# Kernel tuning notes

Measured on AMD Instinct MI355X. Metric: run time of the kernel, lower is better.

Reference implementation:

```python
import jax, jax.numpy as jnp
import numpy as np

TOP_K = 8
EPS = 1e-12  # F.normalize eps


def setup_inputs() -> dict:
    key = jax.random.key(0)
    ks = jax.random.split(key, 16)
    B, C, T, E, H, O, N = 1024, 64, 2, 512, 512, 1, 200000
    f = lambda k, s, scale: jax.random.normal(k, s, jnp.float32) * scale
    z = lambda s: jnp.zeros(s, jnp.float32)
    return {
        "treatment": f(ks[0], (B, T), 1.0),
        "confounders": f(ks[1], (B, C), 1.0),
        "patient": f(ks[2], (B, C + T), 1.0),
        "corpus_embeddings": f(ks[3], (N, E), 1.0),
        "W_pe": f(ks[4], (C + T, E), 0.05), "b_pe": z((E,)),
        "W_te": f(ks[5], (T, H), 0.05), "b_te": z((H,)),
        "W_ce": f(ks[6], (C, H), 0.05), "b_ce": z((H,)),
        "W_re": f(ks[7], (E * TOP_K, H), 0.02), "b_re": z((H,)),
        "W_o1": f(ks[8], (3 * H, H), 0.02), "b_o1": z((H,)),
        "W_o2": f(ks[9], (H, H // 2), 0.05), "b_o2": z((H // 2,)),
        "W_o3": f(ks[10], (H // 2, O), 0.05), "b_o3": z((O,)),
        "W_p1": f(ks[11], (C, H), 0.05), "b_p1": z((H,)),
        "W_p2": f(ks[12], (H, T), 0.05), "b_p2": z((T,)),
    }


def _l2norm(x):
    # torch F.normalize: x / max(||x||, eps)
    n = jnp.sqrt(jnp.sum(x * x, axis=1, keepdims=True))
    return x / jnp.maximum(n, EPS)


def reference(treatment, confounders, patient, corpus_embeddings,
              W_pe, b_pe, W_te, b_te, W_ce, b_ce, W_re, b_re,
              W_o1, b_o1, W_o2, b_o2, W_o3, b_o3, W_p1, b_p1, W_p2, b_p2):
    B = patient.shape[0]
    # retrieval: encode -> normalize -> similarity -> top-k -> gather
    q = _l2norm(patient @ W_pe + b_pe)                 # [B, E]
    c = _l2norm(corpus_embeddings)                     # [N, E]
    sim = q @ c.T                                      # [B, N]
    scores, idx = jax.lax.top_k(sim, TOP_K)            # [B, K]
    retrieved = corpus_embeddings[idx]                 # [B, K, E] (raw, un-normalized, as in source)
    flat = retrieved.reshape(B, -1)                    # [B, K*E]
    # encoders
    t_enc = treatment @ W_te + b_te
    c_enc = confounders @ W_ce + b_ce
    r_enc = flat @ W_re + b_re
    combined = jnp.concatenate([t_enc, c_enc, r_enc], axis=1)  # [B, 3H]
    # outcome MLP (dropout is identity in eval)
    h = jax.nn.relu(combined @ W_o1 + b_o1)
    h = jax.nn.relu(h @ W_o2 + b_o2)
    outcome = h @ W_o3 + b_o3                          # [B, O]
    # propensity head
    p = jax.nn.relu(confounders @ W_p1 + b_p1)
    propensity = jax.nn.softmax(p @ W_p2 + b_p2, axis=1)
    return outcome, scores, idx, propensity
```

## Files before the change

kernel.cpp:

```cpp
#include <hip/hip_runtime.h>
#include <math.h>

#define TOPK 8
#define NCORPUS 200000
#define BROWS 1024
#define CHUNK 512
#define NCHUNK 391
#define NT 32
#define NPART 4
#define NEGINF (-3.0e38f)

typedef __attribute__((ext_vector_type(8))) short bf16x8;
typedef __attribute__((ext_vector_type(4))) float f32x4;

__device__ __forceinline__ float wave_sum_f32(float v) {
#pragma unroll
  for (int m = 32; m >= 1; m >>= 1) v += __shfl_xor(v, m, 64);
  return v;
}
__device__ __forceinline__ double wave_sum_f64(double v) {
#pragma unroll
  for (int m = 32; m >= 1; m >>= 1) v += __shfl_xor(v, m, 64);
  return v;
}
__device__ __forceinline__ unsigned short f2bf(float f) {
  unsigned int u = __float_as_uint(f);
  unsigned int r = (u + 0x7fffu + ((u >> 16) & 1u)) >> 16;
  return (unsigned short)r;
}
__device__ __forceinline__ void gload16(const void* g, void* l) {
  __builtin_amdgcn_global_load_lds(
      (const __attribute__((address_space(1))) unsigned int*)g,
      (__attribute__((address_space(3))) unsigned int*)l, 16, 0, 0);
}
__device__ __forceinline__ void kins4f(float (&S)[4], float v) {
#pragma unroll
  for (int p = 0; p < 4; ++p) {
    float mx = fmaxf(S[p], v);
    v = fminf(S[p], v);
    S[p] = mx;
  }
}
__device__ __forceinline__ void pmerge4f(float (&a)[4], const float (&b)[4]) {
  float c0 = fmaxf(a[0], b[3]), c1 = fmaxf(a[1], b[2]);
  float c2 = fmaxf(a[2], b[1]), c3 = fmaxf(a[3], b[0]);
  float t;
  t = fmaxf(c0, c2); c2 = fminf(c0, c2); c0 = t;
  t = fmaxf(c1, c3); c3 = fminf(c1, c3); c1 = t;
  t = fmaxf(c0, c1); c1 = fminf(c0, c1); c0 = t;
  t = fmaxf(c2, c3); c3 = fminf(c2, c3); c2 = t;
  a[0] = c0; a[1] = c1; a[2] = c2; a[3] = c3;
}

__global__ void prep_kernel(const float* __restrict__ corpus, unsigned short* __restrict__ Cpk,
                            const float* __restrict__ patient, const float* __restrict__ Wpe,
                            const float* __restrict__ bpe, double* __restrict__ q64,
                            unsigned short* __restrict__ Qpk) {
  __shared__ float ps[66];
  __shared__ double red[4];
  __shared__ double s_den;
  int tid = threadIdx.x;
  if (blockIdx.x < 50000) {
    int wid = tid >> 6, lane = tid & 63;
    int row = blockIdx.x * 4 + wid;
    if (row >= NCORPUS) return;
    const float4* p = (const float4*)(corpus + (size_t)row * 512);
    float4 a = p[lane * 2], b = p[lane * 2 + 1];
    float s = a.x * a.x + a.y * a.y + a.z * a.z + a.w * a.w +
              b.x * b.x + b.y * b.y + b.z * b.z + b.w * b.w;
    s = wave_sum_f32(s);
    float inv = 1.0f / fmaxf(sqrtf(s), 1e-12f);
    union { unsigned short us[8]; uint4 v; } pk;
    pk.us[0] = f2bf(a.x * inv); pk.us[1] = f2bf(a.y * inv);
    pk.us[2] = f2bf(a.z * inv); pk.us[3] = f2bf(a.w * inv);
    pk.us[4] = f2bf(b.x * inv); pk.us[5] = f2bf(b.y * inv);
    pk.us[6] = f2bf(b.z * inv); pk.us[7] = f2bf(b.w * inv);
    *(uint4*)(Cpk + (size_t)row * 512 + lane * 8) = pk.v;
  } else {
    int b = blockIdx.x - 50000;
    if (tid < 66) ps[tid] = patient[b * 66 + tid];
    __syncthreads();
    double v0 = (double)bpe[tid];
    double v1 = (double)bpe[tid + 256];
    for (int k = 0; k < 66; ++k) {
      double p = (double)ps[k];
      v0 += p * (double)Wpe[k * 512 + tid];
      v1 += p * (double)Wpe[k * 512 + tid + 256];
    }
    double ss = wave_sum_f64(v0 * v0 + v1 * v1);
    if ((tid & 63) == 0) red[tid >> 6] = ss;
    __syncthreads();
    if (tid == 0) s_den = fmax(sqrt(red[0] + red[1] + red[2] + red[3]), 1e-12);
    __syncthreads();
    double den = s_den;
    double o0 = v0 / den, o1 = v1 / den;
    q64[(size_t)b * 512 + tid] = o0;
    q64[(size_t)b * 512 + tid + 256] = o1;
    Qpk[(size_t)b * 512 + tid] = f2bf((float)o0);
    Qpk[(size_t)b * 512 + tid + 256] = f2bf((float)o1);
  }
}

template <bool CHECK>
__device__ __forceinline__ void fold_sub(f32x4 (&acc)[4][4], float (&lk)[4][4],
                                         int tagbase, int rb2) {
#pragma unroll
  for (int m = 0; m < 4; ++m)
#pragma unroll
    for (int j = 0; j < 4; ++j) {
      int mj = m * 16 + j;
      unsigned tg = (unsigned)(tagbase - mj);
      bool ok = true;
      if (CHECK) ok = (rb2 + mj) < NCORPUS;
#pragma unroll
      for (int n = 0; n < 4; ++n) {
        unsigned bb = (__float_as_uint(acc[m][n][j]) & 0xFFFFFC00u) | tg;
        float tf = __uint_as_float(bb);
        if (CHECK) tf = ok ? tf : NEGINF;
        kins4f(lk[n], tf);
      }
    }
}

__global__ __launch_bounds__(256, 2) void sim_topk_mfma(
    const unsigned short* __restrict__ Qpk, const unsigned short* __restrict__ Cpk,
    unsigned int* __restrict__ part_k) {
  __shared__ __align__(16) unsigned short smem[2][16384];

  int tid = threadIdx.x;
  int lane = tid & 63, wid = tid >> 6;
  int wr = wid >> 1, wc = wid & 1;
  int g = (blockIdx.x & 7) * NCHUNK + (blockIdx.x >> 3);
  int chunk = g >> 3, mt = g & 7;
  int m0 = mt * 128;
  int rbase = chunk * CHUNK;
  bool lastChunk = (rbase + CHUNK) > NCORPUS;

  int srow = tid >> 3;
  int scol = (((tid & 7) ^ (srow & 7)) << 3);

  int l15 = lane & 15, l4 = lane >> 4, l7 = lane & 7;
  int aoff[2][4], boff[2][4];
#pragma unroll
  for (int kk = 0; kk < 2; ++kk)
#pragma unroll
    for (int q = 0; q < 4; ++q) {
      int sw = (((kk * 4 + l4) ^ l7) << 3);
      aoff[kk][q] = (wr * 64 + q * 16 + l15) * 64 + sw;
      boff[kk][q] = 8192 + (wc * 64 + q * 16 + l15) * 64 + sw;
    }

  float lk[4][NPART];
#pragma unroll
  for (int n = 0; n < 4; ++n)
#pragma unroll
    for (int p = 0; p < NPART; ++p) lk[n][p] = NEGINF;

  f32x4 zero = {0.f, 0.f, 0.f, 0.f};
  f32x4 acc[4][4];
#pragma unroll
  for (int m = 0; m < 4; ++m)
#pragma unroll
    for (int n = 0; n < 4; ++n) acc[m][n] = zero;

  auto stageA = [&](int t, unsigned short* dst) {
    int sub = t >> 3, kt = t & 7;
    int rb = rbase + sub * 128;
    int k0 = kt * 64;
#pragma unroll
    for (int r = 0; r < 4; ++r) {
      int cr = rb + r * 32 + srow;
      if (cr > NCORPUS - 1) cr = NCORPUS - 1;
      gload16(Cpk + (size_t)cr * 512 + k0 + scol, dst + (r * 4 + wid) * 512);
    }
  };
  auto stageB = [&](int t, unsigned short* dst) {
    int kt = t & 7;
    int k0 = kt * 64;
#pragma unroll
    for (int r = 0; r < 4; ++r) {
      int qr = m0 + r * 32 + srow;
      gload16(Qpk + (size_t)qr * 512 + k0 + scol, dst + 8192 + (r * 4 + wid) * 512);
    }
  };

  stageA(0, smem[0]);
  stageB(0, smem[0]);

  for (int t = 0; t < NT; ++t) {
    int t1 = t + 1;
    if (t1 < NT) {
      unsigned short* nb = smem[t1 & 1];
      stageA(t1, nb);
      stageB(t1, nb);
      asm volatile("s_waitcnt vmcnt(8)" ::: "memory");
    } else {
      asm volatile("s_waitcnt vmcnt(0)" ::: "memory");
    }
    __builtin_amdgcn_s_barrier();
    const unsigned short* cb = smem[t & 1];
#pragma unroll
    for (int kk = 0; kk < 2; ++kk) {
      bf16x8 a[4], b[4];
#pragma unroll
      for (int m = 0; m < 4; ++m) a[m] = *(const bf16x8*)(cb + aoff[kk][m]);
#pragma unroll
      for (int n = 0; n < 4; ++n) b[n] = *(const bf16x8*)(cb + boff[kk][n]);
#pragma unroll
      for (int m = 0; m < 4; ++m)
#pragma unroll
        for (int n = 0; n < 4; ++n)
          acc[m][n] = __builtin_amdgcn_mfma_f32_16x16x32_bf16(a[m], b[n], acc[m][n], 0, 0, 0);
    }
    if ((t & 7) == 7) {
      int sub = t >> 3;
      int cellbase = sub * 128 + wr * 64 + l4 * 4;
      int rb2 = rbase + cellbase;
      int tagbase = (CHUNK - 1) - cellbase;
      if (lastChunk) fold_sub<true>(acc, lk, tagbase, rb2);
      else fold_sub<false>(acc, lk, tagbase, rb2);
#pragma unroll
      for (int m = 0; m < 4; ++m)
#pragma unroll
        for (int n = 0; n < 4; ++n) acc[m][n] = zero;
    }
    __builtin_amdgcn_s_barrier();
  }

#pragma unroll
  for (int rnd = 0; rnd < 2; ++rnd) {
    int msk = 16 << rnd;
#pragma unroll
    for (int n = 0; n < 4; ++n) {
      float ov[NPART];
#pragma unroll
      for (int p = 0; p < NPART; ++p) ov[p] = __shfl_xor(lk[n][p], msk, 64);
      pmerge4f(lk[n], ov);
    }
  }
  float* fb = (float*)&smem[0][0];
  if (wr == 1 && l4 == 0) {
#pragma unroll
    for (int n = 0; n < 4; ++n) {
      int col = wc * 64 + n * 16 + l15;
#pragma unroll
      for (int p = 0; p < NPART; ++p) fb[col * 4 + p] = lk[n][p];
    }
  }
  __syncthreads();
  if (wr == 0 && l4 == 0) {
#pragma unroll
    for (int n = 0; n < 4; ++n) {
      int col = wc * 64 + n * 16 + l15;
      float ov[NPART];
#pragma unroll
      for (int p = 0; p < NPART; ++p) ov[p] = fb[col * 4 + p];
      pmerge4f(lk[n], ov);
      size_t base = ((size_t)(m0 + col) * NCHUNK + chunk) * NPART;
#pragma unroll
      for (int p = 0; p < NPART; ++p) {
        unsigned bits = __float_as_uint(lk[n][p]);
        unsigned tag = bits & 0x3FFu;
        unsigned flip = bits ^ ((unsigned)((int)bits >> 31) | 0x80000000u);
        part_k[base + p] = (flip & 0xFFFFFC00u) | tag;
      }
    }
  }
}

__global__ __launch_bounds__(256, 2) void mr_tp_kernel(
    const unsigned int* __restrict__ part_k,
    const double* __restrict__ q64, const float* __restrict__ corpus,
    float* __restrict__ out_scores, float* __restrict__ out_idxf, int* __restrict__ topidx,
    const float* __restrict__ treatment, const float* __restrict__ conf,
    const float* __restrict__ Wte, const float* __restrict__ bte,
    const float* __restrict__ Wce, const float* __restrict__ bce,
    const float* __restrict__ Wp1, const float* __restrict__ bp1,
    const float* __restrict__ Wp2, const float* __restrict__ bp2,
    float* __restrict__ combined, float* __restrict__ out_prop) {
  __shared__ float cs[64];
  __shared__ float red0[4], red1[4];
  int tid = threadIdx.x;
  if (blockIdx.x < 256) {
    int wv = tid >> 6, lane = tid & 63;
    int row = blockIdx.x * 4 + wv;
    if (row >= BROWS) return;

    unsigned tk[16]; int tm[16];
#pragma unroll
    for (int p = 0; p < 16; ++p) { tk[p] = 0u; tm[p] = 0; }
    const unsigned* base = part_k + (size_t)row * (NCHUNK * NPART);
    for (int e = lane; e < NCHUNK * NPART; e += 64) {
      unsigned k = base[e];
      if (k > tk[15]) {
        unsigned kv = k; int mv = e;
#pragma unroll
        for (int p = 0; p < 16; ++p) {
          bool gt = kv > tk[p];
          unsigned ts = tk[p]; int ti = tm[p];
          tk[p] = gt ? kv : ts; tm[p] = gt ? mv : ti;
          kv = gt ? ts : kv;    mv = gt ? ti : mv;
        }
      }
    }
#pragma unroll
    for (int r = 0; r < 6; ++r) {
      unsigned ov[16]; int om[16];
#pragma unroll
      for (int p = 0; p < 16; ++p) {
        ov[p] = __shfl_xor(tk[p], 1 << r, 64);
        om[p] = __shfl_xor(tm[p], 1 << r, 64);
      }
      unsigned cv[16]; int cm[16];
#pragma unroll
      for (int i = 0; i < 16; ++i) {
        bool t = tk[i] >= ov[15 - i];
        cv[i] = t ? tk[i] : ov[15 - i];
        cm[i] = t ? tm[i] : om[15 - i];
      }
#pragma unroll
      for (int s = 8; s >= 1; s >>= 1)
#pragma unroll
        for (int bb = 0; bb < 16; bb += 2 * s)
#pragma unroll
          for (int o = 0; o < s; ++o) {
            int x = bb + o, y = bb + o + s;
            bool t = cv[x] >= cv[y];
            unsigned hv = t ? cv[x] : cv[y]; unsigned lv = t ? cv[y] : cv[x];
            int hm = t ? cm[x] : cm[y];      int lm = t ? cm[y] : cm[x];
            cv[x] = hv; cm[x] = hm; cv[y] = lv; cm[y] = lm;
          }
#pragma unroll
      for (int i = 0; i < 16; ++i) { tk[i] = cv[i]; tm[i] = cm[i]; }
    }
    int cidx[16];
#pragma unroll
    for (int c = 0; c < 16; ++c) {
      int ic = ((tm[c] >> 2) << 9) + (CHUNK - 1) - (int)(tk[c] & 0x3FFu);
      if (ic > NCORPUS - 1) ic = NCORPUS - 1;
      if (ic < 0) ic = 0;
      cidx[c] = ic;
    }
    double qv[8];
    const double* qrow = q64 + (size_t)row * 512;
#pragma unroll
    for (int t = 0; t < 8; ++t) qv[t] = qrow[lane * 8 + t];
    double rs[16];
#pragma unroll
    for (int c = 0; c < 16; ++c) {
      const float* crow = corpus + (size_t)cidx[c] * 512 + lane * 8;
      double qd = 0.0, cd = 0.0;
#pragma unroll
      for (int t = 0; t < 8; ++t) {
        double x = (double)crow[t];
        cd += x * x;
        qd += qv[t] * x;
      }
      qd = wave_sum_f64(qd);
      cd = wave_sum_f64(cd);
      rs[c] = qd / fmax(sqrt(cd), 1e-12);
    }
    if (lane == 0) {
      for (int o = 0; o < TOPK; ++o) {
        double bsc = -1e300;
        int bid2 = 0x7fffffff, bc = -1;
#pragma unroll
        for (int c = 0; c < 16; ++c) {
          bool better = (rs[c] > bsc) || (rs[c] == bsc && cidx[c] < bid2);
          if (better) { bsc = rs[c]; bid2 = cidx[c]; bc = c; }
        }
        out_scores[row * 8 + o] = (float)bsc;
        out_idxf[row * 8 + o] = (float)bid2;
        topidx[row * 8 + o] = bid2;
#pragma unroll
        for (int c = 0; c < 16; ++c)
          if (c == bc) rs[c] = -1e300;
      }
    }
  } else {
    int b = blockIdx.x - 256;
    if (tid < 64) cs[tid] = conf[b * 64 + tid];
    __syncthreads();
    float t0 = treatment[b * 2], t1 = treatment[b * 2 + 1];
    float l0 = 0.f, l1 = 0.f;
#pragma unroll
    for (int rep = 0; rep < 2; ++rep) {
      int h = tid + rep * 256;
      float te = fmaf(t0, Wte[h], fmaf(t1, Wte[512 + h], bte[h]));
      combined[(size_t)b * 1024 + h] = te;
      float ce = bce[h];
      float pv = bp1[h];
      for (int k = 0; k < 64; ++k) {
        float c = cs[k];
        ce = fmaf(c, Wce[k * 512 + h], ce);
        pv = fmaf(c, Wp1[k * 512 + h], pv);
      }
      combined[(size_t)b * 1024 + 512 + h] = ce;
      pv = fmaxf(pv, 0.f);
      l0 = fmaf(pv, Wp2[h * 2], l0);
      l1 = fmaf(pv, Wp2[h * 2 + 1], l1);
    }
    l0 = wave_sum_f32(l0);
    l1 = wave_sum_f32(l1);
    int wv = tid >> 6, lane = tid & 63;
    if (lane == 0) { red0[wv] = l0; red1[wv] = l1; }
    __syncthreads();
    if (tid == 0) {
      float a = red0[0] + red0[1] + red0[2] + red0[3] + bp2[0];
      float c2 = red1[0] + red1[1] + red1[2] + red1[3] + bp2[1];
      float m = fmaxf(a, c2);
      float e0 = expf(a - m), e1 = expf(c2 - m);
      float inv = 1.f / (e0 + e1);
      out_prop[b * 2] = e0 * inv;
      out_prop[b * 2 + 1] = e1 * inv;
    }
  }
}

template <int MODE, bool SPLIT, bool EPI>
__global__ __launch_bounds__(256, 2) void gemm64_kernel(
    const float* __restrict__ combined, const float* __restrict__ p0,
    const float* __restrict__ p1, const float* __restrict__ abias,
    const int* __restrict__ gidx, const float* __restrict__ corpus,
    const float* __restrict__ W, int ldw, const float* __restrict__ ebias,
    float* __restrict__ C0, float* __restrict__ C1, int ldc, int Kspan) {
  __shared__ float As[2][32 * 68];
  __shared__ float Bs[2][32 * 72];
  __shared__ int gi[512];
  int tid = threadIdx.x;
  int by = blockIdx.y;
  int m0, koff;
  float* Cout;
  if (SPLIT) {
    m0 = (by >> 1) * 64;
    int kh = by & 1;
    koff = kh * Kspan;
    Cout = kh ? C1 : C0;
  } else {
    m0 = by * 64;
    koff = 0;
    Cout = C0;
  }
  int n0 = blockIdx.x * 64;
  int nk = Kspan >> 5;

  if (MODE == 0) {
    gi[tid] = gidx[m0 * 8 + tid];
    gi[tid + 256] = gidx[m0 * 8 + tid + 256];
    __syncthreads();
  }

  int arow0 = tid >> 3, afc = tid & 7;
  int arow1 = arow0 + 32;
  int bkb0 = tid >> 4, bnf = tid & 15;
  int bkb1 = bkb0 + 16;

  auto stageA1 = [&](int row, int ks, int buf) {
    int kg = koff + ks * 32 + afc * 4;
    float4 v;
    if (MODE == 0) {
      int r = gi[row * 8 + (kg >> 9)];
      v = *(const float4*)(corpus + (size_t)r * 512 + (kg & 511));
    } else if (MODE == 1) {
      if (kg < 1024) {
        v = *(const float4*)(combined + (size_t)(m0 + row) * 1024 + kg);
      } else {
        int e = kg - 1024;
        float4 x = *(const float4*)(p0 + (size_t)(m0 + row) * 512 + e);
        float4 y = *(const float4*)(p1 + (size_t)(m0 + row) * 512 + e);
        float4 z = *(const float4*)(abias + e);
        v.x = x.x + y.x + z.x; v.y = x.y + y.y + z.y;
        v.z = x.z + y.z + z.z; v.w = x.w + y.w + z.w;
      }
    } else {
      float4 x = *(const float4*)(p0 + (size_t)(m0 + row) * 512 + kg);
      float4 y = *(const float4*)(p1 + (size_t)(m0 + row) * 512 + kg);
      float4 z = *(const float4*)(abias + kg);
      v.x = fmaxf(x.x + y.x + z.x, 0.f); v.y = fmaxf(x.y + y.y + z.y, 0.f);
      v.z = fmaxf(x.z + y.z + z.z, 0.f); v.w = fmaxf(x.w + y.w + z.w, 0.f);
    }
    float* d = As[buf] + (afc * 4) * 68 + row;
    d[0] = v.x; d[68] = v.y; d[136] = v.z; d[204] = v.w;
  };
  auto stage = [&](int ks, int buf) {
    stageA1(arow0, ks, buf);
    stageA1(arow1, ks, buf);
    int kg0 = koff + ks * 32 + bkb0;
    *(float4*)(Bs[buf] + bkb0 * 72 + bnf * 4) =
        *(const float4*)(W + (size_t)kg0 * ldw + n0 + bnf * 4);
    int kg1 = koff + ks * 32 + bkb1;
    *(float4*)(Bs[buf] + bkb1 * 72 + bnf * 4) =
        *(const float4*)(W + (size_t)kg1 * ldw + n0 + bnf * 4);
  };

  float acc[4][4];
#pragma unroll
  for (int i = 0; i < 4; ++i)
#pragma unroll
    for (int j = 0; j < 4; ++j) acc[i][j] = 0.f;

  int tm = tid >> 4, tn = tid & 15;

  stage(0, 0);
  __syncthreads();
  for (int ks = 0; ks < nk; ++ks) {
    if (ks + 1 < nk) stage(ks + 1, (ks + 1) & 1);
    const float* as = As[ks & 1];
    const float* bs = Bs[ks & 1];
#pragma unroll
    for (int k = 0; k < 32; ++k) {
      float4 a4 = *(const float4*)(as + k * 68 + tm * 4);
      float4 b4 = *(const float4*)(bs + k * 72 + tn * 4);
      float av[4] = {a4.x, a4.y, a4.z, a4.w};
      float bv[4] = {b4.x, b4.y, b4.z, b4.w};
#pragma unroll
      for (int i = 0; i < 4; ++i)
#pragma unroll
        for (int j = 0; j < 4; ++j) acc[i][j] = fmaf(av[i], bv[j], acc[i][j]);
    }
    __syncthreads();
  }

  float4 eb = make_float4(0.f, 0.f, 0.f, 0.f);
  if (EPI) eb = *(const float4*)(ebias + n0 + tn * 4);
#pragma unroll
  for (int i = 0; i < 4; ++i) {
    float4 v;
    v.x = acc[i][0]; v.y = acc[i][1]; v.z = acc[i][2]; v.w = acc[i][3];
    if (EPI) {
      v.x = fmaxf(v.x + eb.x, 0.f); v.y = fmaxf(v.y + eb.y, 0.f);
      v.z = fmaxf(v.z + eb.z, 0.f); v.w = fmaxf(v.w + eb.w, 0.f);
    }
    *(float4*)(Cout + (size_t)(m0 + tm * 4 + i) * ldc + n0 + tn * 4) = v;
  }
}

__global__ void outcome_kernel(const float* __restrict__ h2, const float* __restrict__ Wo3,
                               const float* __restrict__ bo3, float* __restrict__ out) {
  int wv = threadIdx.x >> 6, lane = threadIdx.x & 63;
  int row = blockIdx.x * 4 + wv;
  if (row >= BROWS) return;
  float4 a = ((const float4*)(h2 + (size_t)row * 256))[lane];
  float4 w = ((const float4*)Wo3)[lane];
  float s = a.x * w.x + a.y * w.y + a.z * w.z + a.w * w.w;
  s = wave_sum_f32(s);
  if (lane == 0) out[row] = s + bo3[0];
}

extern "C" void kernel_launch(void* const* d_in, const int* in_sizes, int n_in,
                              void* d_out, int out_size, void* d_ws, size_t ws_size,
                              hipStream_t stream) {
  const float* treatment = (const float*)d_in[0];
  const float* conf = (const float*)d_in[1];
  const float* patient = (const float*)d_in[2];
  const float* corpus = (const float*)d_in[3];
  const float* Wpe = (const float*)d_in[4];
  const float* bpe = (const float*)d_in[5];
  const float* Wte = (const float*)d_in[6];
  const float* bte = (const float*)d_in[7];
  const float* Wce = (const float*)d_in[8];
  const float* bce = (const float*)d_in[9];
  const float* Wre = (const float*)d_in[10];
  const float* bre = (const float*)d_in[11];
  const float* Wo1 = (const float*)d_in[12];
  const float* bo1 = (const float*)d_in[13];
  const float* Wo2 = (const float*)d_in[14];
  const float* bo2 = (const float*)d_in[15];
  const float* Wo3 = (const float*)d_in[16];
  const float* bo3 = (const float*)d_in[17];
  const float* Wp1 = (const float*)d_in[18];
  const float* bp1 = (const float*)d_in[19];
  const float* Wp2 = (const float*)d_in[20];
  const float* bp2 = (const float*)d_in[21];

  float* out = (float*)d_out;
  float* out_outcome = out;
  float* out_scores = out + 1024;
  float* out_idxf = out + 1024 + 8192;
  float* out_prop = out + 1024 + 8192 + 8192;

  char* ws = (char*)d_ws;
  size_t off = 0;
  auto carve = [&](size_t bytes) {
    void* p = ws + off;
    off = (off + bytes + 255) & ~(size_t)255;
    return p;
  };
  double* q64 = (double*)carve((size_t)1024 * 512 * 8);
  unsigned short* Qpk = (unsigned short*)carve((size_t)1024 * 512 * 2);
  unsigned short* Cpk = (unsigned short*)carve((size_t)NCORPUS * 512 * 2);
  unsigned int* part_k = (unsigned int*)carve((size_t)1024 * NCHUNK * NPART * 4);
  int* topidx = (int*)carve((size_t)1024 * 8 * 4);
  float* combined = (float*)carve((size_t)1024 * 1024 * 4);
  float* p0 = (float*)carve((size_t)1024 * 512 * 4);
  float* p1 = (float*)carve((size_t)1024 * 512 * 4);
  float* pp0 = (float*)carve((size_t)1024 * 512 * 4);
  float* pp1 = (float*)carve((size_t)1024 * 512 * 4);
  float* h2 = (float*)carve((size_t)1024 * 256 * 4);

  prep_kernel<<<dim3(51024), dim3(256), 0, stream>>>(corpus, Cpk, patient, Wpe, bpe, q64, Qpk);
  sim_topk_mfma<<<dim3(8 * NCHUNK), dim3(256), 0, stream>>>(Qpk, Cpk, part_k);
  mr_tp_kernel<<<dim3(1280), dim3(256), 0, stream>>>(part_k, q64, corpus,
                                                     out_scores, out_idxf, topidx,
                                                     treatment, conf, Wte, bte, Wce, bce,
                                                     Wp1, bp1, Wp2, bp2, combined, out_prop);
  gemm64_kernel<0, true, false><<<dim3(8, 32), dim3(256), 0, stream>>>(
      (const float*)nullptr, (const float*)nullptr, (const float*)nullptr, (const float*)nullptr,
      topidx, corpus, Wre, 512, (const float*)nullptr, p0, p1, 512, 2048);
  gemm64_kernel<1, true, false><<<dim3(8, 32), dim3(256), 0, stream>>>(
      combined, p0, p1, bre, (const int*)nullptr, (const float*)nullptr,
      Wo1, 512, (const float*)nullptr, pp0, pp1, 512, 768);
  gemm64_kernel<2, false, true><<<dim3(4, 16), dim3(256), 0, stream>>>(
      (const float*)nullptr, pp0, pp1, bo1, (const int*)nullptr, (const float*)nullptr,
      Wo2, 256, bo2, h2, (float*)nullptr, 256, 512);
  outcome_kernel<<<dim3(256), dim3(256), 0, stream>>>(h2, Wo3, bo3, out_outcome);
}
```

Measured before the change: 635.6 us.

## Compute retrieval encoder with bf16 MFMA using normalized corpus and norm rescale

```diff
diff --git a/kernel.cpp b/kernel.cpp
--- a/kernel.cpp
+++ b/kernel.cpp
@@ -55,10 +55,12 @@
 __global__ void prep_kernel(const float* __restrict__ corpus, unsigned short* __restrict__ Cpk,
                             const float* __restrict__ patient, const float* __restrict__ Wpe,
                             const float* __restrict__ bpe, double* __restrict__ q64,
-                            unsigned short* __restrict__ Qpk) {
+                            unsigned short* __restrict__ Qpk,
+                            const float* __restrict__ Wre, unsigned short* __restrict__ WreT) {
   __shared__ float ps[66];
   __shared__ double red[4];
   __shared__ double s_den;
+  __shared__ float tbuf[64 * 65];
   int tid = threadIdx.x;
   if (blockIdx.x < 50000) {
     int wid = tid >> 6, lane = tid & 63;
@@ -76,7 +78,7 @@
     pk.us[4] = f2bf(b.x * inv); pk.us[5] = f2bf(b.y * inv);
     pk.us[6] = f2bf(b.z * inv); pk.us[7] = f2bf(b.w * inv);
     *(uint4*)(Cpk + (size_t)row * 512 + lane * 8) = pk.v;
-  } else {
+  } else if (blockIdx.x < 51024) {
     int b = blockIdx.x - 50000;
     if (tid < 66) ps[tid] = patient[b * 66 + tid];
     __syncthreads();
@@ -98,6 +100,25 @@
     q64[(size_t)b * 512 + tid + 256] = o1;
     Qpk[(size_t)b * 512 + tid] = f2bf((float)o0);
     Qpk[(size_t)b * 512 + tid + 256] = f2bf((float)o1);
+  } else {
+    int tb = blockIdx.x - 51024;
+    int kt = tb >> 3, nt = tb & 7;
+    int k0 = kt * 64, n0 = nt * 64;
+    int r = tid >> 2, q = tid & 3;
+#pragma unroll
+    for (int i = 0; i < 4; ++i) {
+      float4 v = *(const float4*)(Wre + (size_t)(k0 + r) * 512 + n0 + q * 16 + i * 4);
+      float* d = tbuf + r * 65 + q * 16 + i * 4;
+      d[0] = v.x; d[1] = v.y; d[2] = v.z; d[3] = v.w;
+    }
+    __syncthreads();
+    int n = tid >> 2, s = tid & 3;
+    union { unsigned short us[16]; uint4 v[2]; } ob;
+#pragma unroll
+    for (int j = 0; j < 16; ++j) ob.us[j] = f2bf(tbuf[(s * 16 + j) * 65 + n]);
+    unsigned short* dst = WreT + (size_t)(n0 + n) * 4096 + k0 + s * 16;
+    *(uint4*)dst = ob.v[0];
+    *(uint4*)(dst + 8) = ob.v[1];
   }
 }
 
@@ -272,6 +293,7 @@
     const unsigned int* __restrict__ part_k,
     const double* __restrict__ q64, const float* __restrict__ corpus,
     float* __restrict__ out_scores, float* __restrict__ out_idxf, int* __restrict__ topidx,
+    float* __restrict__ rnorm,
     const float* __restrict__ treatment, const float* __restrict__ conf,
     const float* __restrict__ Wte, const float* __restrict__ bte,
     const float* __restrict__ Wce, const float* __restrict__ bce,
@@ -346,6 +368,7 @@
 #pragma unroll
     for (int t = 0; t < 8; ++t) qv[t] = qrow[lane * 8 + t];
     double rs[16];
+    float rn[16];
 #pragma unroll
     for (int c = 0; c < 16; ++c) {
       const float* crow = corpus + (size_t)cidx[c] * 512 + lane * 8;
@@ -358,7 +381,9 @@
       }
       qd = wave_sum_f64(qd);
       cd = wave_sum_f64(cd);
-      rs[c] = qd / fmax(sqrt(cd), 1e-12);
+      double nr = fmax(sqrt(cd), 1e-12);
+      rs[c] = qd / nr;
+      rn[c] = (float)nr;
     }
     if (lane == 0) {
       for (int o = 0; o < TOPK; ++o) {
@@ -372,6 +397,7 @@
         out_scores[row * 8 + o] = (float)bsc;
         out_idxf[row * 8 + o] = (float)bid2;
         topidx[row * 8 + o] = bid2;
+        rnorm[row * 8 + o] = rn[bc];
 #pragma unroll
         for (int c = 0; c < 16; ++c)
           if (c == bc) rs[c] = -1e300;
@@ -387,7 +413,7 @@
     for (int rep = 0; rep < 2; ++rep) {
       int h = tid + rep * 256;
       float te = fmaf(t0, Wte[h], fmaf(t1, Wte[512 + h], bte[h]));
-      combined[(size_t)b * 1024 + h] = te;
+      combined[(size_t)b * 1536 + h] = te;
       float ce = bce[h];
       float pv = bp1[h];
       for (int k = 0; k < 64; ++k) {
@@ -395,7 +421,7 @@
         ce = fmaf(c, Wce[k * 512 + h], ce);
         pv = fmaf(c, Wp1[k * 512 + h], pv);
       }
-      combined[(size_t)b * 1024 + 512 + h] = ce;
+      combined[(size_t)b * 1536 + 512 + h] = ce;
       pv = fmaxf(pv, 0.f);
       l0 = fmaf(pv, Wp2[h * 2], l0);
       l1 = fmaf(pv, Wp2[h * 2 + 1], l1);
@@ -417,38 +443,141 @@
   }
 }
 
-template <int MODE, bool SPLIT, bool EPI>
-__global__ __launch_bounds__(256, 2) void gemm64_kernel(
-    const float* __restrict__ combined, const float* __restrict__ p0,
-    const float* __restrict__ p1, const float* __restrict__ abias,
-    const int* __restrict__ gidx, const float* __restrict__ corpus,
-    const float* __restrict__ W, int ldw, const float* __restrict__ ebias,
+__global__ __launch_bounds__(256, 1) void renc_mfma(
+    const unsigned short* __restrict__ Cpk, const unsigned short* __restrict__ WreT,
+    const int* __restrict__ topidx, const float* __restrict__ rnorm,
+    const float* __restrict__ bre, float* __restrict__ combined) {
+  __shared__ __align__(16) unsigned short smem[2][16384];
+  __shared__ int gi[1024];
+
+  int tid = threadIdx.x;
+  int lane = tid & 63, wid = tid >> 6;
+  int wr = wid >> 1, wc = wid & 1;
+  int m0 = (blockIdx.x >> 2) * 128;
+  int n0 = (blockIdx.x & 3) * 128;
+
+#pragma unroll
+  for (int i = 0; i < 4; ++i) gi[tid + i * 256] = topidx[m0 * 8 + tid + i * 256];
+  __syncthreads();
+
+  int srow = tid >> 3;
+  int scol = (((tid & 7) ^ (srow & 7)) << 3);
+  int idxr[4][8];
+#pragma unroll
+  for (int r = 0; r < 4; ++r)
+#pragma unroll
+    for (int s = 0; s < 8; ++s) idxr[r][s] = gi[(r * 32 + srow) * 8 + s];
+
+  int l15 = lane & 15, l4 = lane >> 4, l7 = lane & 7;
+  int aoff[2][4], boff[2][4];
+#pragma unroll
+  for (int kk = 0; kk < 2; ++kk)
+#pragma unroll
+    for (int q = 0; q < 4; ++q) {
+      int sw = (((kk * 4 + l4) ^ l7) << 3);
+      aoff[kk][q] = (wr * 64 + q * 16 + l15) * 64 + sw;
+      boff[kk][q] = 8192 + (wc * 64 + q * 16 + l15) * 64 + sw;
+    }
+
+  f32x4 zero = {0.f, 0.f, 0.f, 0.f};
+  f32x4 acc[4][4], acc2[4][4];
+#pragma unroll
+  for (int m = 0; m < 4; ++m)
+#pragma unroll
+    for (int n = 0; n < 4; ++n) { acc[m][n] = zero; acc2[m][n] = zero; }
+
+  auto stageA = [&](int t, unsigned short* dst) {
+    int seg = t >> 3;
+    int kk = (t & 7) * 64;
+#pragma unroll
+    for (int r = 0; r < 4; ++r)
+      gload16(Cpk + (size_t)idxr[r][seg] * 512 + kk + scol, dst + (r * 4 + wid) * 512);
+  };
+  auto stageB = [&](int t, unsigned short* dst) {
+    int k0 = t * 64;
+#pragma unroll
+    for (int r = 0; r < 4; ++r) {
+      int nr = n0 + r * 32 + srow;
+      gload16(WreT + (size_t)nr * 4096 + k0 + scol, dst + 8192 + (r * 4 + wid) * 512);
+    }
+  };
+
+  stageA(0, smem[0]);
+  stageB(0, smem[0]);
+
+  for (int t = 0; t < 64; ++t) {
+    int t1 = t + 1;
+    if (t1 < 64) {
+      unsigned short* nb = smem[t1 & 1];
+      stageA(t1, nb);
+      stageB(t1, nb);
+      asm volatile("s_waitcnt vmcnt(8)" ::: "memory");
+    } else {
+      asm volatile("s_waitcnt vmcnt(0)" ::: "memory");
+    }
+    __builtin_amdgcn_s_barrier();
+    const unsigned short* cb = smem[t & 1];
+#pragma unroll
+    for (int kk = 0; kk < 2; ++kk) {
+      bf16x8 a[4], b[4];
+#pragma unroll
+      for (int m = 0; m < 4; ++m) a[m] = *(const bf16x8*)(cb + aoff[kk][m]);
+#pragma unroll
+      for (int n = 0; n < 4; ++n) b[n] = *(const bf16x8*)(cb + boff[kk][n]);
+#pragma unroll
+      for (int m = 0; m < 4; ++m)
+#pragma unroll
+        for (int n = 0; n < 4; ++n)
+          acc[m][n] = __builtin_amdgcn_mfma_f32_16x16x32_bf16(a[m], b[n], acc[m][n], 0, 0, 0);
+    }
+    if ((t & 7) == 7) {
+      int seg = t >> 3;
+#pragma unroll
+      for (int m = 0; m < 4; ++m)
+#pragma unroll
+        for (int j = 0; j < 4; ++j) {
+          int row = m0 + wr * 64 + m * 16 + l4 * 4 + j;
+          float rn = rnorm[row * 8 + seg];
+#pragma unroll
+          for (int n = 0; n < 4; ++n) acc2[m][n][j] = fmaf(rn, acc[m][n][j], acc2[m][n][j]);
+        }
+#pragma unroll
+      for (int m = 0; m < 4; ++m)
+#pragma unroll
+        for (int n = 0; n < 4; ++n) acc[m][n] = zero;
+    }
+    __builtin_amdgcn_s_barrier();
+  }
+
+#pragma unroll
+  for (int m = 0; m < 4; ++m)
+#pragma unroll
+    for (int j = 0; j < 4; ++j) {
+      int row = m0 + wr * 64 + m * 16 + l4 * 4 + j;
+#pragma unroll
+      for (int n = 0; n < 4; ++n) {
+        int col = n0 + wc * 64 + n * 16 + l15;
+        combined[(size_t)row * 1536 + 1024 + col] = acc2[m][n][j] + bre[col];
+      }
+    }
+}
+
+template <bool RELUIN>
+__global__ __launch_bounds__(256, 2) void gemm64f(
+    const float* __restrict__ A, int lda,
+    const float* __restrict__ p0, const float* __restrict__ p1, const float* __restrict__ ab,
+    const float* __restrict__ W, int ldw,
     float* __restrict__ C0, float* __restrict__ C1, int ldc, int Kspan) {
   __shared__ float As[2][32 * 68];
   __shared__ float Bs[2][32 * 72];
-  __shared__ int gi[512];
   int tid = threadIdx.x;
   int by = blockIdx.y;
-  int m0, koff;
-  float* Cout;
-  if (SPLIT) {
-    m0 = (by >> 1) * 64;
-    int kh = by & 1;
-    koff = kh * Kspan;
-    Cout = kh ? C1 : C0;
-  } else {
-    m0 = by * 64;
-    koff = 0;
-    Cout = C0;
-  }
+  int m0 = (by >> 1) * 64;
+  int kh = by & 1;
+  int koff = kh * Kspan;
+  float* Cout = kh ? C1 : C0;
   int n0 = blockIdx.x * 64;
   int nk = Kspan >> 5;
-
-  if (MODE == 0) {
-    gi[tid] = gidx[m0 * 8 + tid];
-    gi[tid + 256] = gidx[m0 * 8 + tid + 256];
-    __syncthreads();
-  }
 
   int arow0 = tid >> 3, afc = tid & 7;
   int arow1 = arow0 + 32;
@@ -458,26 +587,14 @@
   auto stageA1 = [&](int row, int ks, int buf) {
     int kg = koff + ks * 32 + afc * 4;
     float4 v;
-    if (MODE == 0) {
-      int r = gi[row * 8 + (kg >> 9)];
-      v = *(const float4*)(corpus + (size_t)r * 512 + (kg & 511));
-    } else if (MODE == 1) {
-      if (kg < 1024) {
-        v = *(const float4*)(combined + (size_t)(m0 + row) * 1024 + kg);
-      } else {
-        int e = kg - 1024;
-        float4 x = *(const float4*)(p0 + (size_t)(m0 + row) * 512 + e);
-        float4 y = *(const float4*)(p1 + (size_t)(m0 + row) * 512 + e);
-        float4 z = *(const float4*)(abias + e);
-        v.x = x.x + y.x + z.x; v.y = x.y + y.y + z.y;
-        v.z = x.z + y.z + z.z; v.w = x.w + y.w + z.w;
-      }
-    } else {
+    if (RELUIN) {
       float4 x = *(const float4*)(p0 + (size_t)(m0 + row) * 512 + kg);
       float4 y = *(const float4*)(p1 + (size_t)(m0 + row) * 512 + kg);
-      float4 z = *(const float4*)(abias + kg);
+      float4 z = *(const float4*)(ab + kg);
       v.x = fmaxf(x.x + y.x + z.x, 0.f); v.y = fmaxf(x.y + y.y + z.y, 0.f);
       v.z = fmaxf(x.z + y.z + z.z, 0.f); v.w = fmaxf(x.w + y.w + z.w, 0.f);
+    } else {
+      v = *(const float4*)(A + (size_t)(m0 + row) * lda + kg);
     }
     float* d = As[buf] + (afc * 4) * 68 + row;
     d[0] = v.x; d[68] = v.y; d[136] = v.z; d[204] = v.w;
@@ -521,28 +638,29 @@
     __syncthreads();
   }
 
-  float4 eb = make_float4(0.f, 0.f, 0.f, 0.f);
-  if (EPI) eb = *(const float4*)(ebias + n0 + tn * 4);
 #pragma unroll
   for (int i = 0; i < 4; ++i) {
     float4 v;
     v.x = acc[i][0]; v.y = acc[i][1]; v.z = acc[i][2]; v.w = acc[i][3];
-    if (EPI) {
-      v.x = fmaxf(v.x + eb.x, 0.f); v.y = fmaxf(v.y + eb.y, 0.f);
-      v.z = fmaxf(v.z + eb.z, 0.f); v.w = fmaxf(v.w + eb.w, 0.f);
-    }
     *(float4*)(Cout + (size_t)(m0 + tm * 4 + i) * ldc + n0 + tn * 4) = v;
   }
 }
 
-__global__ void outcome_kernel(const float* __restrict__ h2, const float* __restrict__ Wo3,
+__global__ void outcome_kernel(const float* __restrict__ h2p0, const float* __restrict__ h2p1,
+                               const float* __restrict__ bo2, const float* __restrict__ Wo3,
                                const float* __restrict__ bo3, float* __restrict__ out) {
   int wv = threadIdx.x >> 6, lane = threadIdx.x & 63;
   int row = blockIdx.x * 4 + wv;
   if (row >= BROWS) return;
-  float4 a = ((const float4*)(h2 + (size_t)row * 256))[lane];
+  float4 a = ((const float4*)(h2p0 + (size_t)row * 256))[lane];
+  float4 b = ((const float4*)(h2p1 + (size_t)row * 256))[lane];
+  float4 c = ((const float4*)bo2)[lane];
   float4 w = ((const float4*)Wo3)[lane];
-  float s = a.x * w.x + a.y * w.y + a.z * w.z + a.w * w.w;
+  float h0 = fmaxf(a.x + b.x + c.x, 0.f);
+  float h1 = fmaxf(a.y + b.y + c.y, 0.f);
+  float h2 = fmaxf(a.z + b.z + c.z, 0.f);
+  float h3 = fmaxf(a.w + b.w + c.w, 0.f);
+  float s = h0 * w.x + h1 * w.y + h2 * w.z + h3 * w.w;
   s = wave_sum_f32(s);
   if (lane == 0) out[row] = s + bo3[0];
 }
@@ -589,29 +707,29 @@
   double* q64 = (double*)carve((size_t)1024 * 512 * 8);
   unsigned short* Qpk = (unsigned short*)carve((size_t)1024 * 512 * 2);
   unsigned short* Cpk = (unsigned short*)carve((size_t)NCORPUS * 512 * 2);
+  unsigned short* WreT = (unsigned short*)carve((size_t)512 * 4096 * 2);
   unsigned int* part_k = (unsigned int*)carve((size_t)1024 * NCHUNK * NPART * 4);
   int* topidx = (int*)carve((size_t)1024 * 8 * 4);
-  float* combined = (float*)carve((size_t)1024 * 1024 * 4);
-  float* p0 = (float*)carve((size_t)1024 * 512 * 4);
-  float* p1 = (float*)carve((size_t)1024 * 512 * 4);
+  float* rnorm = (float*)carve((size_t)1024 * 8 * 4);
+  float* combined = (float*)carve((size_t)1024 * 1536 * 4);
   float* pp0 = (float*)carve((size_t)1024 * 512 * 4);
   float* pp1 = (float*)carve((size_t)1024 * 512 * 4);
-  float* h2 = (float*)carve((size_t)1024 * 256 * 4);
-
-  prep_kernel<<<dim3(51024), dim3(256), 0, stream>>>(corpus, Cpk, patient, Wpe, bpe, q64, Qpk);
+  float* h2p0 = (float*)carve((size_t)1024 * 256 * 4);
+  float* h2p1 = (float*)carve((size_t)1024 * 256 * 4);
+
+  prep_kernel<<<dim3(51536), dim3(256), 0, stream>>>(corpus, Cpk, patient, Wpe, bpe, q64, Qpk,
+                                                     Wre, WreT);
   sim_topk_mfma<<<dim3(8 * NCHUNK), dim3(256), 0, stream>>>(Qpk, Cpk, part_k);
   mr_tp_kernel<<<dim3(1280), dim3(256), 0, stream>>>(part_k, q64, corpus,
-                                                     out_scores, out_idxf, topidx,
+                                                     out_scores, out_idxf, topidx, rnorm,
                                                      treatment, conf, Wte, bte, Wce, bce,
                                                      Wp1, bp1, Wp2, bp2, combined, out_prop);
-  gemm64_kernel<0, true, false><<<dim3(8, 32), dim3(256), 0, stream>>>(
-      (const float*)nullptr, (const float*)nullptr, (const float*)nullptr, (const float*)nullptr,
-      topidx, corpus, Wre, 512, (const float*)nullptr, p0, p1, 512, 2048);
-  gemm64_kernel<1, true, false><<<dim3(8, 32), dim3(256), 0, stream>>>(
-      combined, p0, p1, bre, (const int*)nullptr, (const float*)nullptr,
-      Wo1, 512, (const float*)nullptr, pp0, pp1, 512, 768);
-  gemm64_kernel<2, false, true><<<dim3(4, 16), dim3(256), 0, stream>>>(
-      (const float*)nullptr, pp0, pp1, bo1, (const int*)nullptr, (const float*)nullptr,
-      Wo2, 256, bo2, h2, (float*)nullptr, 256, 512);
-  outcome_kernel<<<dim3(256), dim3(256), 0, stream>>>(h2, Wo3, bo3, out_outcome);
-}
+  renc_mfma<<<dim3(32), dim3(256), 0, stream>>>(Cpk, WreT, topidx, rnorm, bre, combined);
+  gemm64f<false><<<dim3(8, 32), dim3(256), 0, stream>>>(
+      combined, 1536, (const float*)nullptr, (const float*)nullptr, (const float*)nullptr,
+      Wo1, 512, pp0, pp1, 512, 768);
+  gemm64f<true><<<dim3(4, 32), dim3(256), 0, stream>>>(
+      (const float*)nullptr, 0, pp0, pp1, bo1,
+      Wo2, 256, h2p0, h2p1, 256, 256);
+  outcome_kernel<<<dim3(256), dim3(256), 0, stream>>>(h2p0, h2p1, bo2, Wo3, bo3, out_outcome);
+}
```

After: 577.6 us, median of 2. 9.1% less time.
